# Kernel optimization log

Measured on AMD Instinct MI355X. Metric: run time of the kernel, lower is better.

The kernel has to match this reference:

```python
import jax, jax.numpy as jnp
import numpy as np

N = 500000
IN_C = 128
OUT_C = 128


def setup_inputs() -> dict:
    key = jax.random.key(0)
    k1, k2, k3, k4 = jax.random.split(key, 4)
    x = jax.random.normal(k1, (N, IN_C), dtype=jnp.float32)
    # E must equal N for the original `out + out[col]` broadcast to be valid
    edge_index = jax.random.randint(k2, (2, N), 0, N, dtype=jnp.int64)
    # Linear(in_channels, out_channels): W [out, in], b [out]
    bound = 1.0 / np.sqrt(IN_C)
    W = jax.random.uniform(k3, (OUT_C, IN_C), dtype=jnp.float32, minval=-bound, maxval=bound)
    b = jax.random.uniform(k4, (OUT_C,), dtype=jnp.float32, minval=-bound, maxval=bound)
    return {"x": x, "edge_index": edge_index, "W": W, "b": b}


def reference(x, edge_index, W, b):
    row, col = edge_index[0], edge_index[1]
    out = x @ W.T + b                      # [N, C] dense projection
    # gather rows by col, then scatter-add +1 at positions row (duplicates accumulate)
    agg = out[col].at[row].add(jnp.float32(1.0))  # [E, C], E == N
    return out + agg
```

## Files before the change

kernel.cpp:

```cpp
#include <hip/hip_runtime.h>
#include <hip/hip_bf16.h>
#include <stdint.h>

typedef __attribute__((ext_vector_type(8))) __bf16 bf16x8;
typedef __attribute__((ext_vector_type(4))) float floatx4;

#define C 128
#define BROWS 128
#define LSTR 136

__device__ __forceinline__ __bf16 f2b(float f) {
  return __builtin_bit_cast(__bf16, __float2bfloat16(f));
}

__global__ void prep_kernel(const int* __restrict__ rowidx, const float* __restrict__ W,
                            int* __restrict__ deg, __bf16* __restrict__ Wb, int n) {
  int i = blockIdx.x * blockDim.x + threadIdx.x;
  if (i < C * C) Wb[i] = f2b(W[i]);
  if (i < n) atomicAdd(deg + rowidx[i], 1);
}

__launch_bounds__(512, 8)
__global__ void gconv_kernel(const float* __restrict__ x,
                             const int* __restrict__ colidx,
                             const __bf16* __restrict__ Wb,
                             const float* __restrict__ bias,
                             const int* __restrict__ deg,
                             float* __restrict__ out, int n) {
  __shared__ __bf16 sW[C * LSTR];

  const int t = threadIdx.x;
  const int lane = t & 63, w = t >> 6;
  const int l15 = lane & 15, quad = lane >> 4;

  const int base = blockIdx.x * BROWS + w * 16;

  int ga  = base + l15;
  int gal = ga < n ? ga : n - 1;
  int cg  = colidx[gal];

  int gr  = base + quad * 4;
  int grl = (gr + 3 < n) ? gr : ((n - 4) & ~3);
  int4 d4 = *(const int4*)(deg + grl);

  {
    int r = t >> 2, q = t & 3;
    const float4* src = (const float4*)(Wb + r * C + q * 32);
    float4* dst = (float4*)(sW + r * LSTR + q * 32);
#pragma unroll
    for (int i = 0; i < 4; i++) dst[i] = src[i];
  }

  float b2[8];
#pragma unroll
  for (int tt = 0; tt < 8; tt++) b2[tt] = 2.0f * bias[tt * 16 + l15];

  __syncthreads();

  const float4* pa = (const float4*)(x + (size_t)gal * C + quad * 8);
  const float4* pc = (const float4*)(x + (size_t)cg  * C + quad * 8);
  float4 va[8], vc[8];
#pragma unroll
  for (int kc = 0; kc < 4; kc++) {
    va[2 * kc]     = pa[kc * 8];
    va[2 * kc + 1] = pa[kc * 8 + 1];
    vc[2 * kc]     = pc[kc * 8];
    vc[2 * kc + 1] = pc[kc * 8 + 1];
  }

  const __bf16* bB = sW + l15 * LSTR + quad * 8;

  floatx4 acc[8];
#pragma unroll
  for (int i = 0; i < 8; i++) acc[i] = (floatx4){0.f, 0.f, 0.f, 0.f};

#pragma unroll
  for (int kc = 0; kc < 4; kc++) {
    float4 a0 = va[2 * kc], a1 = va[2 * kc + 1];
    float4 c0 = vc[2 * kc], c1 = vc[2 * kc + 1];
    bf16x8 av;
    av[0] = f2b(a0.x + c0.x); av[1] = f2b(a0.y + c0.y);
    av[2] = f2b(a0.z + c0.z); av[3] = f2b(a0.w + c0.w);
    av[4] = f2b(a1.x + c1.x); av[5] = f2b(a1.y + c1.y);
    av[6] = f2b(a1.z + c1.z); av[7] = f2b(a1.w + c1.w);
#pragma unroll
    for (int tt = 0; tt < 8; tt++) {
      bf16x8 bv = *(const bf16x8*)(bB + tt * 16 * LSTR + kc * 32);
      acc[tt] = __builtin_amdgcn_mfma_f32_16x16x32_bf16(av, bv, acc[tt], 0, 0, 0);
    }
  }

  float dvf[4];
  dvf[0] = (float)d4.x; dvf[1] = (float)d4.y;
  dvf[2] = (float)d4.z; dvf[3] = (float)d4.w;
#pragma unroll
  for (int r = 0; r < 4; r++) {
    int g = gr + r;
    if (g < n) {
      float* orow = out + (size_t)g * C + l15;
      float dv = dvf[r];
#pragma unroll
      for (int tt = 0; tt < 8; tt++) orow[tt * 16] = acc[tt][r] + b2[tt] + dv;
    }
  }
}

extern "C" void kernel_launch(void* const* d_in, const int* in_sizes, int n_in,
                              void* d_out, int out_size, void* d_ws, size_t ws_size,
                              hipStream_t stream) {
  const float* x    = (const float*)d_in[0];
  const int*   edge = (const int*)d_in[1];
  const float* W    = (const float*)d_in[2];
  const float* bias = (const float*)d_in[3];
  float* out = (float*)d_out;

  const int n = in_sizes[0] / C;

  int* deg = (int*)d_ws;
  size_t wb_off = ((size_t)n * sizeof(int) + 255) & ~(size_t)255;
  __bf16* Wb = (__bf16*)((char*)d_ws + wb_off);

  hipMemsetAsync(deg, 0, (size_t)n * sizeof(int), stream);

  int nb = (n + 255) / 256;
  prep_kernel<<<nb, 256, 0, stream>>>(edge, W, deg, Wb, n);

  int mb = (n + BROWS - 1) / BROWS;
  gconv_kernel<<<mb, 512, 0, stream>>>(x, edge + n, Wb, bias, deg, out, n);
}
```

Measured before the change: 515.6 us.

## Issue x gathers before W staging, use XOR-swizzled LDS and smaller blocks

The gathers of the x rows (own row and col-indexed row) now start before the block barrier, so their latency overlaps with staging W into shared memory. The shared-memory copy of W uses an XOR swizzle on 16-byte chunks in place of row padding, to avoid bank conflicts. Blocks shrink from 512 to 256 threads (64 rows each) with different launch bounds. The trade-off is more blocks, each re-staging the full 32KB W into LDS, and higher register pressure from holding the gathered values across the barrier.

```diff
diff --git a/kernel.cpp b/kernel.cpp
--- a/kernel.cpp
+++ b/kernel.cpp
@@ -6,8 +6,7 @@
 typedef __attribute__((ext_vector_type(4))) float floatx4;
 
 #define C 128
-#define BROWS 128
-#define LSTR 136
+#define BROWS 64
 
 __device__ __forceinline__ __bf16 f2b(float f) {
   return __builtin_bit_cast(__bf16, __float2bfloat16(f));
@@ -20,14 +19,14 @@
   if (i < n) atomicAdd(deg + rowidx[i], 1);
 }
 
-__launch_bounds__(512, 8)
+__launch_bounds__(256, 5)
 __global__ void gconv_kernel(const float* __restrict__ x,
                              const int* __restrict__ colidx,
                              const __bf16* __restrict__ Wb,
                              const float* __restrict__ bias,
                              const int* __restrict__ deg,
                              float* __restrict__ out, int n) {
-  __shared__ __bf16 sW[C * LSTR];
+  __shared__ bf16x8 sW[2048];
 
   const int t = threadIdx.x;
   const int lane = t & 63, w = t >> 6;
@@ -39,55 +38,72 @@
   int gal = ga < n ? ga : n - 1;
   int cg  = colidx[gal];
 
+  {
+    int r = t >> 1, h = t & 1, rx = r & 15;
+    const bf16x8* src = (const bf16x8*)(Wb + r * C) + h * 8;
+    bf16x8 wreg[8];
+#pragma unroll
+    for (int i = 0; i < 8; i++) wreg[i] = src[i];
+#pragma unroll
+    for (int i = 0; i < 8; i++) sW[r * 16 + ((h * 8 + i) ^ rx)] = wreg[i];
+  }
+
+  const float4* pa = (const float4*)(x + (size_t)gal * C + quad * 8);
+  float4 va[8];
+#pragma unroll
+  for (int kc = 0; kc < 4; kc++) {
+    va[2 * kc]     = pa[kc * 8];
+    va[2 * kc + 1] = pa[kc * 8 + 1];
+  }
+  const float4* pc = (const float4*)(x + (size_t)cg * C + quad * 8);
+  float4 vc[8];
+#pragma unroll
+  for (int kc = 0; kc < 4; kc++) {
+    vc[2 * kc]     = pc[kc * 8];
+    vc[2 * kc + 1] = pc[kc * 8 + 1];
+  }
+
   int gr  = base + quad * 4;
   int grl = (gr + 3 < n) ? gr : ((n - 4) & ~3);
   int4 d4 = *(const int4*)(deg + grl);
-
-  {
-    int r = t >> 2, q = t & 3;
-    const float4* src = (const float4*)(Wb + r * C + q * 32);
-    float4* dst = (float4*)(sW + r * LSTR + q * 32);
-#pragma unroll
-    for (int i = 0; i < 4; i++) dst[i] = src[i];
-  }
 
   float b2[8];
 #pragma unroll
   for (int tt = 0; tt < 8; tt++) b2[tt] = 2.0f * bias[tt * 16 + l15];
 
+  __builtin_amdgcn_sched_barrier(0);
   __syncthreads();
 
-  const float4* pa = (const float4*)(x + (size_t)gal * C + quad * 8);
-  const float4* pc = (const float4*)(x + (size_t)cg  * C + quad * 8);
-  float4 va[8], vc[8];
+  bf16x8 av[4];
 #pragma unroll
   for (int kc = 0; kc < 4; kc++) {
-    va[2 * kc]     = pa[kc * 8];
-    va[2 * kc + 1] = pa[kc * 8 + 1];
-    vc[2 * kc]     = pc[kc * 8];
-    vc[2 * kc + 1] = pc[kc * 8 + 1];
+    float4 a0 = va[2 * kc], a1 = va[2 * kc + 1];
+    float4 c0 = vc[2 * kc], c1 = vc[2 * kc + 1];
+    av[kc][0] = f2b(a0.x + c0.x); av[kc][1] = f2b(a0.y + c0.y);
+    av[kc][2] = f2b(a0.z + c0.z); av[kc][3] = f2b(a0.w + c0.w);
+    av[kc][4] = f2b(a1.x + c1.x); av[kc][5] = f2b(a1.y + c1.y);
+    av[kc][6] = f2b(a1.z + c1.z); av[kc][7] = f2b(a1.w + c1.w);
   }
 
-  const __bf16* bB = sW + l15 * LSTR + quad * 8;
+  int sx0 = (quad + 0)  ^ l15;
+  int sx1 = (quad + 4)  ^ l15;
+  int sx2 = (quad + 8)  ^ l15;
+  int sx3 = (quad + 12) ^ l15;
 
   floatx4 acc[8];
 #pragma unroll
   for (int i = 0; i < 8; i++) acc[i] = (floatx4){0.f, 0.f, 0.f, 0.f};
 
+  const bf16x8* wr0 = sW + l15 * 16 + sx0;
+  const bf16x8* wr1 = sW + l15 * 16 + sx1;
+  const bf16x8* wr2 = sW + l15 * 16 + sx2;
+  const bf16x8* wr3 = sW + l15 * 16 + sx3;
 #pragma unroll
-  for (int kc = 0; kc < 4; kc++) {
-    float4 a0 = va[2 * kc], a1 = va[2 * kc + 1];
-    float4 c0 = vc[2 * kc], c1 = vc[2 * kc + 1];
-    bf16x8 av;
-    av[0] = f2b(a0.x + c0.x); av[1] = f2b(a0.y + c0.y);
-    av[2] = f2b(a0.z + c0.z); av[3] = f2b(a0.w + c0.w);
-    av[4] = f2b(a1.x + c1.x); av[5] = f2b(a1.y + c1.y);
-    av[6] = f2b(a1.z + c1.z); av[7] = f2b(a1.w + c1.w);
-#pragma unroll
-    for (int tt = 0; tt < 8; tt++) {
-      bf16x8 bv = *(const bf16x8*)(bB + tt * 16 * LSTR + kc * 32);
-      acc[tt] = __builtin_amdgcn_mfma_f32_16x16x32_bf16(av, bv, acc[tt], 0, 0, 0);
-    }
+  for (int tt = 0; tt < 8; tt++) {
+    acc[tt] = __builtin_amdgcn_mfma_f32_16x16x32_bf16(av[0], wr0[tt * 256], acc[tt], 0, 0, 0);
+    acc[tt] = __builtin_amdgcn_mfma_f32_16x16x32_bf16(av[1], wr1[tt * 256], acc[tt], 0, 0, 0);
+    acc[tt] = __builtin_amdgcn_mfma_f32_16x16x32_bf16(av[2], wr2[tt * 256], acc[tt], 0, 0, 0);
+    acc[tt] = __builtin_amdgcn_mfma_f32_16x16x32_bf16(av[3], wr3[tt * 256], acc[tt], 0, 0, 0);
   }
 
   float dvf[4];
@@ -126,5 +142,5 @@
   prep_kernel<<<nb, 256, 0, stream>>>(edge, W, deg, Wb, n);
 
   int mb = (n + BROWS - 1) / BROWS;
-  gconv_kernel<<<mb, 512, 0, stream>>>(x, edge + n, Wb, bias, deg, out, n);
+  gconv_kernel<<<mb, 256, 0, stream>>>(x, edge + n, Wb, bias, deg, out, n);
 }
```

New measurement: 508.4 us. About the same (-1.4%).
